# Performance work log

Hardware: AMD Instinct MI355X
Metric: run time of the kernel (lower is better)

## Reference

```python
import jax, jax.numpy as jnp
import numpy as np

N_HEADS = 16


def setup_inputs() -> dict:
    key = jax.random.key(0)
    k1, k2, k3, k4 = jax.random.split(key, 4)
    B, W, c, C = 4, 1024, 32, 1024
    x = jax.random.normal(k1, (B, W, c, C), dtype=jnp.float32)
    w_pos_emb = jax.random.normal(k2, (W, C), dtype=jnp.float32)
    attn_w = jax.random.normal(k3, (3 * C, C), dtype=jnp.float32) * (1.0 / np.sqrt(C))
    proj_w = jax.random.normal(k4, (C, C), dtype=jnp.float32) * (1.0 / np.sqrt(C))
    attention_mask = jnp.ones((B, W, c), dtype=jnp.int32)
    return {"x": x, "w_pos_emb": w_pos_emb, "attn_w": attn_w,
            "proj_w": proj_w, "attention_mask": attention_mask}


def reference(x, w_pos_emb, attn_w, proj_w, attention_mask):
    B, W, c, C = x.shape
    H = N_HEADS
    Dh = C // H
    # last-token pooling: one-hot of (count-1) over char axis, multiply-sum
    last_ix = attention_mask.sum(-1) - 1                      # [B, W]
    oh = jax.nn.one_hot(last_ix, c, dtype=x.dtype)            # [B, W, c]
    word = jnp.einsum('bwcd,bwc->bwd', x, oh)                 # [B, W, C]
    word = word + w_pos_emb                                   # first_time pos-emb add
    # QKV projection (torch Linear: y = x @ W^T)
    qkv = jnp.einsum('bwd,ed->bwe', word, attn_w)             # [B, W, 3C]
    q, k, v = jnp.split(qkv, 3, axis=-1)
    def heads(t):
        return t.reshape(B, W, H, Dh).transpose(0, 2, 1, 3)   # [B, H, W, Dh]
    q, k, v = heads(q), heads(k), heads(v)
    scale = 1.0 / np.sqrt(Dh).astype(np.float32)
    scores = jnp.einsum('bhqd,bhkd->bhqk', q, k) * scale      # [B, H, W, W]
    causal = jnp.tril(jnp.ones((W, W), dtype=bool))
    scores = jnp.where(causal, scores, jnp.finfo(scores.dtype).min)
    probs = jax.nn.softmax(scores, axis=-1)
    out = jnp.einsum('bhqk,bhkd->bhqd', probs, v)             # [B, H, W, Dh]
    out = out.transpose(0, 2, 1, 3).reshape(B, W, C)
    out = jnp.einsum('bwd,ed->bwe', out, proj_w)              # c_proj
    # dropout is identity in eval mode
    return (word, out)
```

## Files before the change

kernel.cpp:

```cpp
#include <hip/hip_runtime.h>

#define BB 4
#define WW 1024
#define CDIM 1024
#define CCH 32
#define NH 16
#define DH 64
#define MROWS (BB * WW)

typedef __bf16 bf16x8 __attribute__((ext_vector_type(8)));
typedef float f32x4 __attribute__((ext_vector_type(4)));

static __device__ __forceinline__ unsigned short f2bf(float f) {
    union { float f; unsigned u; } v; v.f = f;
    unsigned r = v.u + 0x7fffu + ((v.u >> 16) & 1u);
    return (unsigned short)(r >> 16);
}

#if defined(__has_builtin)
#if __has_builtin(__builtin_amdgcn_global_load_lds)
#define HAVE_GLL 1
#endif
#endif

#ifdef HAVE_GLL
static __device__ __forceinline__ void gload16(const void* g, void* l) {
    __builtin_amdgcn_global_load_lds(
        (const __attribute__((address_space(1))) unsigned int*)g,
        (__attribute__((address_space(3))) unsigned int*)l, 16, 0, 0);
}
#endif

__global__ __launch_bounds__(256) void convw_kernel(const float* __restrict__ aw,
                                                    const float* __restrict__ pw,
                                                    unsigned short* __restrict__ awb,
                                                    unsigned short* __restrict__ pwb) {
    int g = blockIdx.x * 256 + threadIdx.x;
    const int NA4 = 3 * CDIM * CDIM / 4;
    if (g < NA4) {
        float4 vv = ((const float4*)aw)[g];
        ushort4 o = { f2bf(vv.x), f2bf(vv.y), f2bf(vv.z), f2bf(vv.w) };
        ((ushort4*)awb)[g] = o;
    } else {
        int k = g - NA4;
        float4 vv = ((const float4*)pw)[k];
        ushort4 o = { f2bf(vv.x), f2bf(vv.y), f2bf(vv.z), f2bf(vv.w) };
        ((ushort4*)pwb)[k] = o;
    }
}

__global__ __launch_bounds__(256) void pool_kernel(const float* __restrict__ x,
                                                   const float* __restrict__ pos,
                                                   const int* __restrict__ mask,
                                                   float* __restrict__ word_f32,
                                                   unsigned short* __restrict__ word_bf) {
    int bw = blockIdx.x;
    int w = bw & (WW - 1);
    __shared__ int s_last;
    if (threadIdx.x == 0) {
        int ssum = 0;
        for (int j = 0; j < CCH; ++j) ssum += mask[bw * CCH + j];
        s_last = ssum - 1;
    }
    __syncthreads();
    int last = s_last;
    const float4* xr = (const float4*)(x + ((size_t)bw * CCH + (last < 0 ? 0 : last)) * CDIM);
    const float4* pr = (const float4*)(pos + (size_t)w * CDIM);
    int d4 = threadIdx.x;
    float4 xv = (last >= 0) ? xr[d4] : float4{0.f, 0.f, 0.f, 0.f};
    float4 pv = pr[d4];
    float4 vv = { xv.x + pv.x, xv.y + pv.y, xv.z + pv.z, xv.w + pv.w };
    ((float4*)(word_f32 + (size_t)bw * CDIM))[d4] = vv;
    ushort4 o = { f2bf(vv.x), f2bf(vv.y), f2bf(vv.z), f2bf(vv.w) };
    ((ushort4*)(word_bf + (size_t)bw * CDIM))[d4] = o;
}

template <int EPI, int BM, int BN, int WRN, int WCN, int MI, int NI>
__global__ __launch_bounds__(256) void gemm_nt_kernel(const unsigned short* __restrict__ A,
                                                      const unsigned short* __restrict__ Bt,
                                                      int Mdim, int Ndim, int Kdim,
                                                      unsigned short* __restrict__ qb,
                                                      unsigned short* __restrict__ kb,
                                                      unsigned short* __restrict__ vb,
                                                      float* __restrict__ outp) {
    __shared__ unsigned short As[BM * 64];
    __shared__ unsigned short Bs[BN * 64];
    int t = threadIdx.x;
    int wid = t >> 6, lane = t & 63;
    int wr = wid / WCN, wc = wid % WCN;
    int mbase = blockIdx.y * BM, nbase = blockIdx.x * BN;
    int lr = lane & 15, lg = lane >> 4;
    f32x4 acc[MI][NI] = {};

#ifdef HAVE_GLL
    int csrc = ((lane & 7) ^ (lane >> 3)) * 8;
    int rofs = lane >> 3;
    const int TOT = (BM + BN) / 8;
#endif

    for (int kt = 0; kt < Kdim; kt += 64) {
        __syncthreads();
#ifdef HAVE_GLL
        for (int c = wid; c < TOT; c += 4) {
            if (c < BM / 8)
                gload16(A + (size_t)(mbase + c * 8 + rofs) * Kdim + kt + csrc, &As[c * 8 * 64]);
            else {
                int cb = c - BM / 8;
                gload16(Bt + (size_t)(nbase + cb * 8 + rofs) * Kdim + kt + csrc, &Bs[cb * 8 * 64]);
            }
        }
#else
        for (int s = 0; s < (BM + BN) / 32; ++s) {
            int f = s * 256 + t;
            int row = f >> 3, c8 = (f & 7) * 8;
            if (row < BM)
                *(int4*)&As[row * 64 + (c8 ^ ((row & 7) << 3))] =
                    *(const int4*)&A[(size_t)(mbase + row) * Kdim + kt + c8];
            else {
                int rb = row - BM;
                *(int4*)&Bs[rb * 64 + (c8 ^ ((rb & 7) << 3))] =
                    *(const int4*)&Bt[(size_t)(nbase + rb) * Kdim + kt + c8];
            }
        }
#endif
        __syncthreads();
        for (int ks = 0; ks < 2; ++ks) {
            bf16x8 af[MI], bfr[NI];
            int cc = ks * 32 + lg * 8;
            for (int mi = 0; mi < MI; ++mi) {
                int r = wr * (MI * 16) + mi * 16 + lr;
                af[mi] = *(const bf16x8*)&As[r * 64 + (cc ^ ((r & 7) << 3))];
            }
            for (int ni = 0; ni < NI; ++ni) {
                int r = wc * (NI * 16) + ni * 16 + lr;
                bfr[ni] = *(const bf16x8*)&Bs[r * 64 + (cc ^ ((r & 7) << 3))];
            }
            __builtin_amdgcn_s_setprio(1);
            for (int mi = 0; mi < MI; ++mi)
                for (int ni = 0; ni < NI; ++ni)
                    acc[mi][ni] = __builtin_amdgcn_mfma_f32_16x16x32_bf16(af[mi], bfr[ni], acc[mi][ni], 0, 0, 0);
            __builtin_amdgcn_s_setprio(0);
        }
    }
    for (int mi = 0; mi < MI; ++mi)
        for (int ni = 0; ni < NI; ++ni)
            for (int i = 0; i < 4; ++i) {
                int row = mbase + wr * (MI * 16) + mi * 16 + lg * 4 + i;
                int col = nbase + wc * (NI * 16) + ni * 16 + lr;
                float v = acc[mi][ni][i];
                if (EPI == 0) {
                    int sect = col >> 10, ch = col & 1023, hh = ch >> 6, dd = ch & 63;
                    int bI = row >> 10, wI = row & 1023;
                    size_t dst = ((size_t)(bI * NH + hh) * WW + wI) * DH + dd;
                    if (sect == 0) qb[dst] = f2bf(v * 0.125f);
                    else if (sect == 1) kb[dst] = f2bf(v);
                    else vb[dst] = f2bf(v);
                } else {
                    outp[(size_t)row * Ndim + col] = v;
                }
            }
}

__global__ __launch_bounds__(512) void attn_kernel(const unsigned short* __restrict__ q,
                                                   const unsigned short* __restrict__ k,
                                                   const unsigned short* __restrict__ v,
                                                   unsigned short* __restrict__ aout) {
    __shared__ unsigned short Ks[64 * 64];
    __shared__ unsigned short Vt[64 * 64];
    __shared__ unsigned short Ps0[128 * 64];
    __shared__ unsigned short Ps1[128 * 64];
    int t = threadIdx.x;
    int wid = t >> 6, lane = t & 63;
    int lr = lane & 15, lg = lane >> 4;
    int bh = blockIdx.y, bI = bh >> 4, hI = bh & 15;
    int p = blockIdx.x;
    int qa = p * 128, qbv = (7 - p) * 128;
    int nktA = 2 * p + 2, nktB = 16 - 2 * p;

    bf16x8 qfA[2], qfB[2];
    {
        const unsigned short* qg = q + (size_t)bh * WW * DH;
        int r = wid * 16 + lr;
        for (int ks = 0; ks < 2; ++ks) {
            qfA[ks] = *(const bf16x8*)&qg[(size_t)(qa + r) * DH + ks * 32 + lg * 8];
            qfB[ks] = *(const bf16x8*)&qg[(size_t)(qbv + r) * DH + ks * 32 + lg * 8];
        }
    }

    float rmA[4], rlA[4], rmB[4], rlB[4];
    f32x4 oA[4] = {}, oB[4] = {};
    for (int i = 0; i < 4; ++i) { rmA[i] = rmB[i] = -1e30f; rlA[i] = rlB[i] = 0.f; }

    const unsigned short* kbase = k + (size_t)bh * WW * DH;
    const unsigned short* vbase = v + (size_t)bh * WW * DH;
    int dp = (t & 31) * 2, kb8 = (t >> 5) & 7;
    int tt = t & 255;
    int krow = tt >> 3, kc8 = (tt & 7) * 8;

    unsigned int vr[8]; int4 kr0, kr1;
    auto prefetch = [&](int tn) {
        if (wid < 4) {
            const unsigned short* vg = vbase + (size_t)tn * 64 * DH;
#pragma unroll
            for (int j = 0; j < 8; ++j)
                vr[j] = *(const unsigned int*)&vg[(size_t)(kb8 * 8 + j) * DH + dp];
        } else {
            const unsigned short* kg = kbase + (size_t)tn * 64 * DH;
            kr0 = *(const int4*)&kg[(size_t)krow * DH + kc8];
            kr1 = *(const int4*)&kg[(size_t)(krow + 32) * DH + kc8];
        }
    };
    prefetch(0);

    auto process = [&](const bf16x8* qf, int qbase, float* rm, float* rl, f32x4* o,
                       unsigned short* PsX, int tki) {
        f32x4 s[4] = {};
        for (int ks = 0; ks < 2; ++ks) {
            bf16x8 bfr[4];
            int cc = ks * 32 + lg * 8;
            for (int ni = 0; ni < 4; ++ni) {
                int r = ni * 16 + lr;
                bfr[ni] = *(const bf16x8*)&Ks[r * 64 + (cc ^ ((r & 7) << 3))];
            }
            __builtin_amdgcn_s_setprio(1);
            for (int ni = 0; ni < 4; ++ni)
                s[ni] = __builtin_amdgcn_mfma_f32_16x16x32_bf16(qf[ks], bfr[ni], s[ni], 0, 0, 0);
            __builtin_amdgcn_s_setprio(0);
        }
        int rowbase = qbase + wid * 16 + lg * 4;
        if (tki * 64 + 63 > qbase + wid * 16) {
            for (int ni = 0; ni < 4; ++ni)
                for (int i = 0; i < 4; ++i) {
                    int ki = tki * 64 + ni * 16 + lr;
                    if (ki > rowbase + i) s[ni][i] = -1e30f;
                }
        }
        for (int i = 0; i < 4; ++i) {
            float mx = fmaxf(fmaxf(s[0][i], s[1][i]), fmaxf(s[2][i], s[3][i]));
            for (int d = 8; d >= 1; d >>= 1) mx = fmaxf(mx, __shfl_xor(mx, d));
            float mnew = fmaxf(rm[i], mx);
            float sf = __expf(rm[i] - mnew);
            float psum = 0.f;
            for (int ni = 0; ni < 4; ++ni) {
                float pe = __expf(s[ni][i] - mnew);
                s[ni][i] = pe;
                psum += pe;
            }
            for (int d = 8; d >= 1; d >>= 1) psum += __shfl_xor(psum, d);
            rl[i] = rl[i] * sf + psum;
            rm[i] = mnew;
            for (int di = 0; di < 4; ++di) o[di][i] *= sf;
        }
        for (int ni = 0; ni < 4; ++ni)
            for (int i = 0; i < 4; ++i) {
                int r = wid * 16 + lg * 4 + i;
                PsX[r * 64 + ((ni * 16 + lr) ^ ((r & 7) << 3))] = f2bf(s[ni][i]);
            }
    };

    auto pvacc = [&](f32x4* o, const unsigned short* PsX) {
        for (int ks = 0; ks < 2; ++ks) {
            int cc = ks * 32 + lg * 8;
            int r = wid * 16 + lr;
            bf16x8 pa = *(const bf16x8*)&PsX[r * 64 + (cc ^ ((r & 7) << 3))];
            bf16x8 vbf[4];
            for (int di = 0; di < 4; ++di) {
                int rv = di * 16 + lr;
                vbf[di] = *(const bf16x8*)&Vt[rv * 64 + (cc ^ ((rv & 7) << 3))];
            }
            __builtin_amdgcn_s_setprio(1);
            for (int di = 0; di < 4; ++di)
                o[di] = __builtin_amdgcn_mfma_f32_16x16x32_bf16(pa, vbf[di], o[di], 0, 0, 0);
            __builtin_amdgcn_s_setprio(0);
        }
    };

    for (int tki = 0; tki < nktB; ++tki) {
        __syncthreads();
        if (wid < 4) {
            unsigned short lo[8], hi[8];
#pragma unroll
            for (int j = 0; j < 8; ++j) { lo[j] = (unsigned short)(vr[j] & 0xffffu);
                                          hi[j] = (unsigned short)(vr[j] >> 16); }
            *(int4*)&Vt[dp * 64 + ((kb8 * 8) ^ ((dp & 7) << 3))] = *(int4*)lo;
            int d1 = dp + 1;
            *(int4*)&Vt[d1 * 64 + ((kb8 * 8) ^ ((d1 & 7) << 3))] = *(int4*)hi;
        } else {
            *(int4*)&Ks[krow * 64 + (kc8 ^ ((krow & 7) << 3))] = kr0;
            int r1 = krow + 32;
            *(int4*)&Ks[r1 * 64 + (kc8 ^ ((r1 & 7) << 3))] = kr1;
        }
        if (tki + 1 < nktB) prefetch(tki + 1);
        __syncthreads();

        bool actA = (tki < nktA);
        bool wB = (tki * 64 <= qbv + wid * 16 + 15);
        bool wA = actA && (tki * 64 <= qa + wid * 16 + 15);
        if (wB) process(qfB, qbv, rmB, rlB, oB, Ps1, tki);
        if (wA) process(qfA, qa, rmA, rlA, oA, Ps0, tki);
        __syncthreads();
        if (wB) pvacc(oB, Ps1);
        if (wA) pvacc(oA, Ps0);
    }

    for (int di = 0; di < 4; ++di)
        for (int i = 0; i < 4; ++i) {
            int dd = di * 16 + lr;
            int qrA = qa + wid * 16 + lg * 4 + i;
            int qrB = qbv + wid * 16 + lg * 4 + i;
            aout[((size_t)bI * WW + qrA) * CDIM + hI * DH + dd] = f2bf(oA[di][i] / rlA[i]);
            aout[((size_t)bI * WW + qrB) * CDIM + hI * DH + dd] = f2bf(oB[di][i] / rlB[i]);
        }
}

extern "C" void kernel_launch(void* const* d_in, const int* in_sizes, int n_in,
                              void* d_out, int out_size, void* d_ws, size_t ws_size,
                              hipStream_t stream) {
    const float* x    = (const float*)d_in[0];
    const float* pos  = (const float*)d_in[1];
    const float* aw   = (const float*)d_in[2];
    const float* pw   = (const float*)d_in[3];
    const int*   mask = (const int*)d_in[4];
    float* out = (float*)d_out;
    float* word_f32 = out;
    float* proj_out = out + (size_t)MROWS * CDIM;

    const size_t MB = 1u << 20;
    char* ws = (char*)d_ws;
    unsigned short* word_bf = (unsigned short*)(ws);
    unsigned short* awb     = (unsigned short*)(ws + 8 * MB);
    unsigned short* pwb     = (unsigned short*)(ws + 14 * MB);
    unsigned short* qb      = (unsigned short*)(ws + 16 * MB);
    unsigned short* kb      = (unsigned short*)(ws + 24 * MB);
    unsigned short* vb      = (unsigned short*)(ws + 32 * MB);
    unsigned short* aob     = (unsigned short*)(ws + 40 * MB);

    convw_kernel<<<4096, 256, 0, stream>>>(aw, pw, awb, pwb);
    pool_kernel<<<MROWS, 256, 0, stream>>>(x, pos, mask, word_f32, word_bf);
    gemm_nt_kernel<0, 128, 128, 2, 2, 4, 4><<<dim3(3 * CDIM / 128, MROWS / 128), 256, 0, stream>>>(
        word_bf, awb, MROWS, 3 * CDIM, CDIM, qb, kb, vb, nullptr);
    attn_kernel<<<dim3(4, BB * NH), 512, 0, stream>>>(qb, kb, vb, aob);
    gemm_nt_kernel<1, 128, 64, 4, 1, 2, 4><<<dim3(CDIM / 64, MROWS / 128), 256, 0, stream>>>(
        aob, pwb, MROWS, CDIM, CDIM, nullptr, nullptr, nullptr, proj_out);
}
```

Measured before the change: 114.6 us.

## Add double-buffered 256x192 QKV GEMM kernel and merge prep kernels

Replaces the QKV projection GEMM with a new 512-thread kernel that computes 256x192 tiles. It double-buffers LDS, interleaves async global-to-LDS loads with MFMA phases, and raises wave priority around the MFMA blocks. It also merges the weight-conversion and pooling kernels into a single launch. The intent is to hide load latency and increase data reuse in the dominant GEMM, at the cost of heavy LDS use. A host-side occupancy check picks the new kernel and falls back to the old one.

```diff
diff --git a/kernel.cpp b/kernel.cpp
--- a/kernel.cpp
+++ b/kernel.cpp
@@ -31,49 +31,186 @@
 }
 #endif
 
-__global__ __launch_bounds__(256) void convw_kernel(const float* __restrict__ aw,
-                                                    const float* __restrict__ pw,
-                                                    unsigned short* __restrict__ awb,
-                                                    unsigned short* __restrict__ pwb) {
-    int g = blockIdx.x * 256 + threadIdx.x;
-    const int NA4 = 3 * CDIM * CDIM / 4;
-    if (g < NA4) {
-        float4 vv = ((const float4*)aw)[g];
-        ushort4 o = { f2bf(vv.x), f2bf(vv.y), f2bf(vv.z), f2bf(vv.w) };
-        ((ushort4*)awb)[g] = o;
-    } else {
-        int k = g - NA4;
-        float4 vv = ((const float4*)pw)[k];
-        ushort4 o = { f2bf(vv.x), f2bf(vv.y), f2bf(vv.z), f2bf(vv.w) };
-        ((ushort4*)pwb)[k] = o;
-    }
-}
-
-__global__ __launch_bounds__(256) void pool_kernel(const float* __restrict__ x,
+__global__ __launch_bounds__(256) void prep_kernel(const float* __restrict__ aw,
+                                                   const float* __restrict__ pw,
+                                                   const float* __restrict__ x,
                                                    const float* __restrict__ pos,
                                                    const int* __restrict__ mask,
+                                                   unsigned short* __restrict__ awb,
+                                                   unsigned short* __restrict__ pwb,
                                                    float* __restrict__ word_f32,
                                                    unsigned short* __restrict__ word_bf) {
-    int bw = blockIdx.x;
-    int w = bw & (WW - 1);
-    __shared__ int s_last;
-    if (threadIdx.x == 0) {
-        int ssum = 0;
-        for (int j = 0; j < CCH; ++j) ssum += mask[bw * CCH + j];
-        s_last = ssum - 1;
-    }
-    __syncthreads();
-    int last = s_last;
-    const float4* xr = (const float4*)(x + ((size_t)bw * CCH + (last < 0 ? 0 : last)) * CDIM);
-    const float4* pr = (const float4*)(pos + (size_t)w * CDIM);
-    int d4 = threadIdx.x;
-    float4 xv = (last >= 0) ? xr[d4] : float4{0.f, 0.f, 0.f, 0.f};
-    float4 pv = pr[d4];
-    float4 vv = { xv.x + pv.x, xv.y + pv.y, xv.z + pv.z, xv.w + pv.w };
-    ((float4*)(word_f32 + (size_t)bw * CDIM))[d4] = vv;
-    ushort4 o = { f2bf(vv.x), f2bf(vv.y), f2bf(vv.z), f2bf(vv.w) };
-    ((ushort4*)(word_bf + (size_t)bw * CDIM))[d4] = o;
-}
+    int blk = blockIdx.x;
+    if (blk < 4096) {
+        int g = blk * 256 + threadIdx.x;
+        const int NA4 = 3 * CDIM * CDIM / 4;
+        if (g < NA4) {
+            float4 vv = ((const float4*)aw)[g];
+            ushort4 o = { f2bf(vv.x), f2bf(vv.y), f2bf(vv.z), f2bf(vv.w) };
+            ((ushort4*)awb)[g] = o;
+        } else {
+            int kk = g - NA4;
+            float4 vv = ((const float4*)pw)[kk];
+            ushort4 o = { f2bf(vv.x), f2bf(vv.y), f2bf(vv.z), f2bf(vv.w) };
+            ((ushort4*)pwb)[kk] = o;
+        }
+    } else {
+        int bw = blk - 4096;
+        int w = bw & (WW - 1);
+        __shared__ int s_last;
+        if (threadIdx.x == 0) {
+            int ssum = 0;
+            for (int j = 0; j < CCH; ++j) ssum += mask[bw * CCH + j];
+            s_last = ssum - 1;
+        }
+        __syncthreads();
+        int last = s_last;
+        const float4* xr = (const float4*)(x + ((size_t)bw * CCH + (last < 0 ? 0 : last)) * CDIM);
+        const float4* pr = (const float4*)(pos + (size_t)w * CDIM);
+        int d4 = threadIdx.x;
+        float4 xv = (last >= 0) ? xr[d4] : float4{0.f, 0.f, 0.f, 0.f};
+        float4 pv = pr[d4];
+        float4 vv = { xv.x + pv.x, xv.y + pv.y, xv.z + pv.z, xv.w + pv.w };
+        ((float4*)(word_f32 + (size_t)bw * CDIM))[d4] = vv;
+        ushort4 o = { f2bf(vv.x), f2bf(vv.y), f2bf(vv.z), f2bf(vv.w) };
+        ((ushort4*)(word_bf + (size_t)bw * CDIM))[d4] = o;
+    }
+}
+
+#ifdef HAVE_GLL
+#define NTK 16
+#define BUFS 28672
+__global__ __launch_bounds__(512) void gemm_qkv8_kernel(const unsigned short* __restrict__ A,
+                                                        const unsigned short* __restrict__ Bt,
+                                                        unsigned short* __restrict__ qb,
+                                                        unsigned short* __restrict__ kb,
+                                                        unsigned short* __restrict__ vb) {
+    extern __shared__ unsigned short L[];
+    const int K = 1024;
+    int t = threadIdx.x, wid = t >> 6, lane = t & 63;
+    int wm = wid >> 2, wn = wid & 3;
+    int lr = lane & 15, lg = lane >> 4;
+    int mbase = blockIdx.y * 256, nbase = blockIdx.x * 192;
+    int srow = lane >> 3;
+    int scol = ((lane & 7) ^ (lane >> 3)) * 8;
+
+    const unsigned short* Abase = A + (size_t)(mbase + wid * 8 + srow) * K + scol;
+    const unsigned short* Bbase = Bt + (size_t)(nbase + wid * 8 + srow) * K + scol;
+
+#define STAGE_A(buf, unit, tile) \
+    gload16(Abase + (size_t)(unit) * 64 * K + (tile) * 64, \
+            &L[(buf) * BUFS + (unit) * 4096 + wid * 512])
+#define STAGE_B(buf, unit, tile) \
+    gload16(Bbase + (size_t)(unit) * 64 * K + (tile) * 64, \
+            &L[(buf) * BUFS + 16384 + (unit) * 4096 + wid * 512])
+#define LDA(mi_, ks_) (*(const bf16x8*)&L[c * BUFS + (wm * 128 + (mi_) * 16 + lr) * 64 + \
+                        (((ks_) * 32 + lg * 8) ^ ((lr & 7) << 3))])
+#define LDB(ni_, ks_) (*(const bf16x8*)&L[c * BUFS + 16384 + (wn * 48 + (ni_) * 16 + lr) * 64 + \
+                        (((ks_) * 32 + lg * 8) ^ ((lr & 7) << 3))])
+#define PRE_MFMA() do { __builtin_amdgcn_s_barrier(); \
+    asm volatile("s_waitcnt lgkmcnt(0)" ::: "memory"); \
+    __builtin_amdgcn_sched_barrier(0); \
+    __builtin_amdgcn_s_setprio(1); } while (0)
+#define POST_MFMA() do { __builtin_amdgcn_s_setprio(0); \
+    __builtin_amdgcn_s_barrier(); } while (0)
+
+    f32x4 acc[8][3] = {};
+
+    STAGE_A(0, 0, 0); STAGE_A(0, 1, 0); STAGE_A(0, 2, 0); STAGE_A(0, 3, 0);
+    STAGE_B(0, 0, 0); STAGE_B(0, 1, 0); STAGE_B(0, 2, 0);
+    STAGE_B(1, 0, 1); STAGE_B(1, 1, 1); STAGE_B(1, 2, 1);
+    asm volatile("s_waitcnt vmcnt(3)" ::: "memory");
+    __builtin_amdgcn_s_barrier();
+
+    for (int tk = 0; tk < NTK; ++tk) {
+        int c = tk & 1;
+        bf16x8 bfr[3][2], af[2][2];
+
+#pragma unroll
+        for (int ni = 0; ni < 3; ++ni)
+#pragma unroll
+            for (int ks = 0; ks < 2; ++ks)
+                bfr[ni][ks] = LDB(ni, ks);
+#pragma unroll
+        for (int ks = 0; ks < 2; ++ks) { af[0][ks] = LDA(0, ks); af[1][ks] = LDA(1, ks); }
+        if (tk + 1 < NTK) { STAGE_A(c ^ 1, 0, tk + 1); STAGE_A(c ^ 1, 1, tk + 1); }
+        PRE_MFMA();
+#pragma unroll
+        for (int ni = 0; ni < 3; ++ni)
+#pragma unroll
+            for (int ks = 0; ks < 2; ++ks) {
+                acc[0][ni] = __builtin_amdgcn_mfma_f32_16x16x32_bf16(af[0][ks], bfr[ni][ks], acc[0][ni], 0, 0, 0);
+                acc[1][ni] = __builtin_amdgcn_mfma_f32_16x16x32_bf16(af[1][ks], bfr[ni][ks], acc[1][ni], 0, 0, 0);
+            }
+        POST_MFMA();
+
+#pragma unroll
+        for (int ks = 0; ks < 2; ++ks) { af[0][ks] = LDA(2, ks); af[1][ks] = LDA(3, ks); }
+        if (tk + 1 < NTK) { STAGE_A(c ^ 1, 2, tk + 1); STAGE_A(c ^ 1, 3, tk + 1); }
+        PRE_MFMA();
+#pragma unroll
+        for (int ni = 0; ni < 3; ++ni)
+#pragma unroll
+            for (int ks = 0; ks < 2; ++ks) {
+                acc[2][ni] = __builtin_amdgcn_mfma_f32_16x16x32_bf16(af[0][ks], bfr[ni][ks], acc[2][ni], 0, 0, 0);
+                acc[3][ni] = __builtin_amdgcn_mfma_f32_16x16x32_bf16(af[1][ks], bfr[ni][ks], acc[3][ni], 0, 0, 0);
+            }
+        POST_MFMA();
+
+#pragma unroll
+        for (int ks = 0; ks < 2; ++ks) { af[0][ks] = LDA(4, ks); af[1][ks] = LDA(5, ks); }
+        if (tk + 2 < NTK) { STAGE_B(c, 0, tk + 2); STAGE_B(c, 1, tk + 2); }
+        PRE_MFMA();
+#pragma unroll
+        for (int ni = 0; ni < 3; ++ni)
+#pragma unroll
+            for (int ks = 0; ks < 2; ++ks) {
+                acc[4][ni] = __builtin_amdgcn_mfma_f32_16x16x32_bf16(af[0][ks], bfr[ni][ks], acc[4][ni], 0, 0, 0);
+                acc[5][ni] = __builtin_amdgcn_mfma_f32_16x16x32_bf16(af[1][ks], bfr[ni][ks], acc[5][ni], 0, 0, 0);
+            }
+        POST_MFMA();
+
+#pragma unroll
+        for (int ks = 0; ks < 2; ++ks) { af[0][ks] = LDA(6, ks); af[1][ks] = LDA(7, ks); }
+        if (tk + 2 < NTK) { STAGE_B(c, 2, tk + 2); }
+        PRE_MFMA();
+#pragma unroll
+        for (int ni = 0; ni < 3; ++ni)
+#pragma unroll
+            for (int ks = 0; ks < 2; ++ks) {
+                acc[6][ni] = __builtin_amdgcn_mfma_f32_16x16x32_bf16(af[0][ks], bfr[ni][ks], acc[6][ni], 0, 0, 0);
+                acc[7][ni] = __builtin_amdgcn_mfma_f32_16x16x32_bf16(af[1][ks], bfr[ni][ks], acc[7][ni], 0, 0, 0);
+            }
+        __builtin_amdgcn_s_setprio(0);
+        if (tk + 2 < NTK) { asm volatile("s_waitcnt vmcnt(3)" ::: "memory"); }
+        else              { asm volatile("s_waitcnt vmcnt(0)" ::: "memory"); }
+        __builtin_amdgcn_s_barrier();
+    }
+
+#pragma unroll
+    for (int mi = 0; mi < 8; ++mi)
+#pragma unroll
+        for (int ni = 0; ni < 3; ++ni)
+#pragma unroll
+            for (int i = 0; i < 4; ++i) {
+                int row = mbase + wm * 128 + mi * 16 + lg * 4 + i;
+                int col = nbase + wn * 48 + ni * 16 + lr;
+                float v = acc[mi][ni][i];
+                int sect = col >> 10, ch = col & 1023, hh = ch >> 6, dd = ch & 63;
+                int bI = row >> 10, wI = row & 1023;
+                size_t dst = ((size_t)(bI * NH + hh) * WW + wI) * DH + dd;
+                if (sect == 0) qb[dst] = f2bf(v * 0.125f);
+                else if (sect == 1) kb[dst] = f2bf(v);
+                else vb[dst] = f2bf(v);
+            }
+#undef STAGE_A
+#undef STAGE_B
+#undef LDA
+#undef LDB
+#undef PRE_MFMA
+#undef POST_MFMA
+}
+#endif
 
 template <int EPI, int BM, int BN, int WRN, int WCN, int MI, int NI>
 __global__ __launch_bounds__(256) void gemm_nt_kernel(const unsigned short* __restrict__ A,
@@ -101,11 +238,11 @@
     for (int kt = 0; kt < Kdim; kt += 64) {
         __syncthreads();
 #ifdef HAVE_GLL
-        for (int c = wid; c < TOT; c += 4) {
-            if (c < BM / 8)
-                gload16(A + (size_t)(mbase + c * 8 + rofs) * Kdim + kt + csrc, &As[c * 8 * 64]);
+        for (int cch = wid; cch < TOT; cch += 4) {
+            if (cch < BM / 8)
+                gload16(A + (size_t)(mbase + cch * 8 + rofs) * Kdim + kt + csrc, &As[cch * 8 * 64]);
             else {
-                int cb = c - BM / 8;
+                int cb = cch - BM / 8;
                 gload16(Bt + (size_t)(nbase + cb * 8 + rofs) * Kdim + kt + csrc, &Bs[cb * 8 * 64]);
             }
         }
@@ -293,9 +430,8 @@
         if (tki + 1 < nktB) prefetch(tki + 1);
         __syncthreads();
 
-        bool actA = (tki < nktA);
         bool wB = (tki * 64 <= qbv + wid * 16 + 15);
-        bool wA = actA && (tki * 64 <= qa + wid * 16 + 15);
+        bool wA = (tki < nktA) && (tki * 64 <= qa + wid * 16 + 15);
         if (wB) process(qfB, qbv, rmB, rlB, oB, Ps1, tki);
         if (wA) process(qfA, qa, rmA, rlA, oA, Ps0, tki);
         __syncthreads();
@@ -335,10 +471,32 @@
     unsigned short* vb      = (unsigned short*)(ws + 32 * MB);
     unsigned short* aob     = (unsigned short*)(ws + 40 * MB);
 
-    convw_kernel<<<4096, 256, 0, stream>>>(aw, pw, awb, pwb);
-    pool_kernel<<<MROWS, 256, 0, stream>>>(x, pos, mask, word_f32, word_bf);
+    prep_kernel<<<8192, 256, 0, stream>>>(aw, pw, x, pos, mask, awb, pwb, word_f32, word_bf);
+
+#ifdef HAVE_GLL
+    const int QKV_LDS = (2 * BUFS) * 2 + 64;
+    bool deep = false;
+    {
+        (void)hipFuncSetAttribute((const void*)gemm_qkv8_kernel,
+                                  hipFuncAttributeMaxDynamicSharedMemorySize, QKV_LDS);
+        int nb = 0;
+        hipError_t e = hipOccupancyMaxActiveBlocksPerMultiprocessor(
+            &nb, (const void*)gemm_qkv8_kernel, 512, (size_t)QKV_LDS);
+        deep = (e == hipSuccess && nb >= 1);
+        (void)hipGetLastError();
+    }
+    if (deep) {
+        gemm_qkv8_kernel<<<dim3(3 * CDIM / 192, MROWS / 256), 512, QKV_LDS, stream>>>(
+            word_bf, awb, qb, kb, vb);
+    } else {
+        gemm_nt_kernel<0, 128, 128, 2, 2, 4, 4><<<dim3(3 * CDIM / 128, MROWS / 128), 256, 0, stream>>>(
+            word_bf, awb, MROWS, 3 * CDIM, CDIM, qb, kb, vb, nullptr);
+    }
+#else
     gemm_nt_kernel<0, 128, 128, 2, 2, 4, 4><<<dim3(3 * CDIM / 128, MROWS / 128), 256, 0, stream>>>(
         word_bf, awb, MROWS, 3 * CDIM, CDIM, qb, kb, vb, nullptr);
+#endif
+
     attn_kernel<<<dim3(4, BB * NH), 512, 0, stream>>>(qb, kb, vb, aob);
     gemm_nt_kernel<1, 128, 64, 4, 1, 2, 4><<<dim3(CDIM / 64, MROWS / 128), 256, 0, stream>>>(
         aob, pwb, MROWS, CDIM, CDIM, nullptr, nullptr, nullptr, proj_out);
```

Result: no change. 112.6 us (-1.8%).
